# Optimization experiments

Hardware: AMD Instinct MI355X
Metric: run time of the kernel (lower is better)

## Reference

```python
import jax, jax.numpy as jnp
import numpy as np
import math

D_MODEL = 1024
N_HEADS = 16
D_HEAD = D_MODEL // N_HEADS
B, T = 2, 2048


def setup_inputs() -> dict:
    key = jax.random.key(0)
    ks = jax.random.split(key, 5)
    x = jax.random.normal(ks[0], (B, T, D_MODEL), dtype=jnp.float32)
    W_qkv = jax.random.normal(ks[1], (D_MODEL, 3 * D_MODEL), dtype=jnp.float32) * 0.02
    b_qkv = jnp.zeros((3 * D_MODEL,), dtype=jnp.float32)
    W_g = jax.random.normal(ks[2], (N_HEADS, D_HEAD, D_HEAD), dtype=jnp.float32) * 0.02
    W_out = jax.random.normal(ks[3], (D_MODEL, D_MODEL), dtype=jnp.float32) * 0.02
    b_out = jnp.zeros((D_MODEL,), dtype=jnp.float32)
    return {"x": x, "W_qkv": W_qkv, "b_qkv": b_qkv, "W_g": W_g, "W_out": W_out, "b_out": b_out}


def reference(x, W_qkv, b_qkv, W_g, W_out, b_out):
    b, t, d = x.shape
    h, dh = N_HEADS, D_HEAD
    qkv = x @ W_qkv + b_qkv                         # (B,T,3D)
    q, k, v = jnp.split(qkv, 3, axis=-1)
    # (B,T,D) -> (B,H,T,dh)
    q = q.reshape(b, t, h, dh).transpose(0, 2, 1, 3)
    k = k.reshape(b, t, h, dh).transpose(0, 2, 1, 3)
    v = v.reshape(b, t, h, dh).transpose(0, 2, 1, 3)
    scale = 1.0 / math.sqrt(dh)
    scores = jnp.einsum('bhtd,bhsd->bhts', q, k) * scale   # (B,H,T,T)
    causal = jnp.tril(jnp.ones((t, t), dtype=bool))
    scores = jnp.where(causal, scores, jnp.float32(-jnp.inf))
    attn = jax.nn.softmax(scores, axis=-1)
    # query-conditioned bilinear value gate (applied at each position)
    g = jax.nn.sigmoid(jnp.einsum('bhtd,hde->bhte', q, W_g))  # (B,H,T,dh)
    v = g * v
    out = jnp.einsum('bhts,bhsd->bhtd', attn, v)             # (B,H,T,dh)
    out = out.transpose(0, 2, 1, 3).reshape(b, t, d)
    return out @ W_out + b_out
```

## Files before the change

### kernel.cpp

```cpp
#include <hip/hip_runtime.h>
#include <hip/hip_bf16.h>

typedef unsigned short ushortT;
typedef __bf16 bf16x8 __attribute__((ext_vector_type(8)));
typedef __bf16 bf16x4 __attribute__((ext_vector_type(4)));
typedef float f32x4 __attribute__((ext_vector_type(4)));

#define T_SEQ 2048
#define DH 64
#define NH 16
#define DM 1024
#define TD 3072
#define BATCH 2
#define LOG2E 1.44269504f

#define BARRIER()   asm volatile("s_barrier" ::: "memory")
#define VMCNT(n)    asm volatile("s_waitcnt vmcnt(" #n ")" ::: "memory")

__device__ inline ushortT f2bf(float f){
    union { float f; unsigned int u; } a; a.f = f;
    unsigned int r = a.u + 0x7fffu + ((a.u >> 16) & 1u);
    return (ushortT)(r >> 16);
}
__device__ inline float bf2f(ushortT u){
    union { float f; unsigned int u; } a; a.u = ((unsigned int)u) << 16;
    return a.f;
}

__device__ inline void gload_lds16(const void* g, void* l){
    __builtin_amdgcn_global_load_lds((const __attribute__((address_space(1))) void*)g,
                                     (__attribute__((address_space(3))) void*)l, 16, 0, 0);
}

__global__ __launch_bounds__(256) void cast_bf16_kernel(const float* __restrict__ in,
                                                        ushortT* __restrict__ out, int n){
    int i = (blockIdx.x * 256 + threadIdx.x) * 4;
    if (i < n){
        float4 v = *(const float4*)&in[i];
        out[i+0] = f2bf(v.x); out[i+1] = f2bf(v.y);
        out[i+2] = f2bf(v.z); out[i+3] = f2bf(v.w);
    }
}

__global__ __launch_bounds__(256) void transcast_kernel(const float* __restrict__ in,
                                                        ushortT* __restrict__ out, int K, int N){
    __shared__ float tile[64][65];
    int n0 = blockIdx.x * 64, k0 = blockIdx.y * 64;
    int tid = threadIdx.x;
    int c  = tid & 63;
    int r4 = tid >> 6;
#pragma unroll
    for (int i = 0; i < 16; i++){
        int k = r4 + i * 4;
        tile[k][c] = in[(size_t)(k0 + k) * N + n0 + c];
    }
    __syncthreads();
#pragma unroll
    for (int i = 0; i < 16; i++){
        int n = r4 + i * 4;
        out[(size_t)(n0 + n) * K + k0 + c] = f2bf(tile[c][n]);
    }
}

__global__ __launch_bounds__(256) void wg_transcast_kernel(const float* __restrict__ in,
                                                           ushortT* __restrict__ out){
    __shared__ float tile[64][65];
    int h = blockIdx.x;
    int tid = threadIdx.x;
    int c = tid & 63, r4 = tid >> 6;
#pragma unroll
    for (int i = 0; i < 16; i++){
        int d = r4 + i*4;
        tile[d][c] = in[h*4096 + d*64 + c];
    }
    __syncthreads();
#pragma unroll
    for (int i = 0; i < 16; i++){
        int e = r4 + i*4;
        out[h*4096 + e*64 + c] = f2bf(tile[c][e]);
    }
}

__device__ inline void store_out(ushortT* C, size_t i, float v){ C[i] = f2bf(v); }
__device__ inline void store_out(float*   C, size_t i, float v){ C[i] = v; }

template <typename OUT>
__global__ __launch_bounds__(256) void gemm_bf16_kernel(const ushortT* __restrict__ A,
                                                        const ushortT* __restrict__ BT,
                                                        const float* __restrict__ bias,
                                                        OUT* __restrict__ C,
                                                        int M, int N, int K){
    __shared__ __align__(16) ushortT As[2][128*32];
    __shared__ __align__(16) ushortT Bs[2][128*32];
    int tid = threadIdx.x;
    int m0 = blockIdx.x * 128;
    int n0 = blockIdx.y * 128;
    int wid = tid >> 6, lane = tid & 63;
    int l15 = lane & 15, g = lane >> 4;
    int wr = wid >> 1, wc = wid & 1;

    f32x4 acc[4][4];
#pragma unroll
    for (int i = 0; i < 4; i++)
#pragma unroll
        for (int j = 0; j < 4; j++) acc[i][j] = (f32x4){0.f,0.f,0.f,0.f};

    int srow = wid * 32 + (lane >> 2);
    int sch  = lane & 3;

#define GSTAGE(buf, k0)                                                                  \
    {                                                                                    \
        _Pragma("unroll")                                                                \
        for (int i_ = 0; i_ < 2; i_++){                                                  \
            int row_ = srow + i_ * 16;                                                   \
            const ushortT* asrc_ = A  + (size_t)(m0 + row_) * K + (k0) + sch * 8;        \
            const ushortT* bsrc_ = BT + (size_t)(n0 + row_) * K + (k0) + sch * 8;        \
            gload_lds16(asrc_, (char*)As[buf] + (wid*2 + i_) * 1024);                    \
            gload_lds16(bsrc_, (char*)Bs[buf] + (wid*2 + i_) * 1024);                    \
        }                                                                                \
    }

    GSTAGE(0, 0);

    int nk = K >> 5;
    for (int kt = 0; kt < nk; kt++){
        int buf = kt & 1;
        BARRIER();
        if (kt + 1 < nk){
            GSTAGE(buf ^ 1, (kt + 1) * 32);
            VMCNT(4);
        } else {
            VMCNT(0);
        }
        BARRIER();

        bf16x8 af[4], bfr[4];
#pragma unroll
        for (int mi = 0; mi < 4; mi++){
            int r = wr*64 + mi*16 + l15;
            af[mi]  = *(const bf16x8*)(As[buf] + r*32 + g*8);
        }
#pragma unroll
        for (int ni = 0; ni < 4; ni++){
            int r = wc*64 + ni*16 + l15;
            bfr[ni] = *(const bf16x8*)(Bs[buf] + r*32 + g*8);
        }
#pragma unroll
        for (int mi = 0; mi < 4; mi++)
#pragma unroll
            for (int ni = 0; ni < 4; ni++)
                acc[mi][ni] = __builtin_amdgcn_mfma_f32_16x16x32_bf16(af[mi], bfr[ni], acc[mi][ni], 0, 0, 0);
    }
#undef GSTAGE

#pragma unroll
    for (int mi = 0; mi < 4; mi++){
#pragma unroll
        for (int jj = 0; jj < 4; jj++){
            int mm = m0 + wr*64 + mi*16 + 4*g + jj;
#pragma unroll
            for (int ni = 0; ni < 4; ni++){
                int nn = n0 + wc*64 + ni*16 + l15;
                float v = acc[mi][ni][jj] + bias[nn];
                store_out(C, (size_t)mm * N + nn, v);
            }
        }
    }
}

__global__ __launch_bounds__(256) void gate_kernel(const ushortT* __restrict__ qkv,
                                                   const ushortT* __restrict__ WgT,
                                                   ushortT* __restrict__ vgT){
    __shared__ __align__(16) ushortT VT[64][72];
    int tblk = blockIdx.x, bh = blockIdx.y;
    int b = bh >> 4, h = bh & 15;
    int tid = threadIdx.x, wid = tid >> 6, lane = tid & 63;
    int l15 = lane & 15, g = lane >> 4;
    int t0 = tblk * 64;
    int tl = wid*16 + l15;

    const ushortT* qrow = qkv + ((size_t)b*T_SEQ + t0 + tl)*TD + h*DH;
    bf16x8 qf0 = *(const bf16x8*)(qrow + 8*g);
    bf16x8 qf1 = *(const bf16x8*)(qrow + 32 + 8*g);

    const ushortT* wbase = WgT + h*4096;
    const ushortT* vrow = qkv + ((size_t)b*T_SEQ + t0 + tl)*TD + 2*DM + h*DH;

#pragma unroll
    for (int ns = 0; ns < 4; ns++){
        int e = ns*16 + l15;
        bf16x8 wf0 = *(const bf16x8*)(wbase + e*64 + 8*g);
        bf16x8 wf1 = *(const bf16x8*)(wbase + e*64 + 32 + 8*g);
        f32x4 z = (f32x4){0.f,0.f,0.f,0.f};
        z = __builtin_amdgcn_mfma_f32_16x16x32_bf16(wf0, qf0, z, 0, 0, 0);
        z = __builtin_amdgcn_mfma_f32_16x16x32_bf16(wf1, qf1, z, 0, 0, 0);
        union { ushortT u[4]; uint2 v; } v4;
        v4.v = *(const uint2*)(vrow + ns*16 + 4*g);
#pragma unroll
        for (int jj = 0; jj < 4; jj++){
            float ex = __builtin_amdgcn_exp2f(-z[jj] * LOG2E);
            float gv = __builtin_amdgcn_rcpf(1.f + ex);
            VT[ns*16 + 4*g + jj][tl] = f2bf(gv * bf2f(v4.u[jj]));
        }
    }
    __syncthreads();
    for (int i = tid; i < 64*8; i += 256){
        int e = i >> 3, c8 = (i & 7) * 8;
        *(uint4*)&vgT[((size_t)bh * DH + e) * T_SEQ + t0 + c8] = *(const uint4*)&VT[e][c8];
    }
}

struct QS {
    bf16x8 qf0, qf1;
    float m_, lsum;
    f32x4 acc[4];
};

__device__ __forceinline__ void proc2(const ushortT* __restrict__ K0,
                                      const ushortT* __restrict__ V0,
                                      const ushortT* __restrict__ K1,
                                      const ushortT* __restrict__ V1,
                                      QS& S, int t0, int t1, int myp,
                                      int wq, int l15, int g){
    int l7 = l15 & 7;
    f32x4 s[8];
    __builtin_amdgcn_s_setprio(1);
#pragma unroll
    for (int ns = 0; ns < 4; ns++){
        int kr = ns*16 + l15;
        bf16x8 kf0 = *(const bf16x8*)(K0 + kr*64 + ((g    ) ^ l7)*8);
        bf16x8 kf1 = *(const bf16x8*)(K0 + kr*64 + ((4 + g) ^ l7)*8);
        f32x4 z = (f32x4){0.f,0.f,0.f,0.f};
        z = __builtin_amdgcn_mfma_f32_16x16x32_bf16(kf0, S.qf0, z, 0, 0, 0);
        z = __builtin_amdgcn_mfma_f32_16x16x32_bf16(kf1, S.qf1, z, 0, 0, 0);
        s[ns] = z;
    }
#pragma unroll
    for (int ns = 0; ns < 4; ns++){
        int kr = ns*16 + l15;
        bf16x8 kf0 = *(const bf16x8*)(K1 + kr*64 + ((g    ) ^ l7)*8);
        bf16x8 kf1 = *(const bf16x8*)(K1 + kr*64 + ((4 + g) ^ l7)*8);
        f32x4 z = (f32x4){0.f,0.f,0.f,0.f};
        z = __builtin_amdgcn_mfma_f32_16x16x32_bf16(kf0, S.qf0, z, 0, 0, 0);
        z = __builtin_amdgcn_mfma_f32_16x16x32_bf16(kf1, S.qf1, z, 0, 0, 0);
        s[4 + ns] = z;
    }
    __builtin_amdgcn_s_setprio(0);

    int qrel = wq*16 + l15;
    bool diag0 = (t0 == myp);
    bool inv1  = (t1 > myp);
    bool diag1 = (t1 == myp);
    if (diag0){
#pragma unroll
        for (int ns = 0; ns < 4; ns++){
            int kb = ((ns & 2) << 4) + 8*g + ((ns & 1) << 2);
#pragma unroll
            for (int jj = 0; jj < 4; jj++)
                if (kb + jj > qrel) s[ns][jj] = -INFINITY;
        }
    }
    if (inv1){
#pragma unroll
        for (int ns = 0; ns < 4; ns++)
#pragma unroll
            for (int jj = 0; jj < 4; jj++) s[4+ns][jj] = -INFINITY;
    } else if (diag1){
#pragma unroll
        for (int ns = 0; ns < 4; ns++){
            int kb = ((ns & 2) << 4) + 8*g + ((ns & 1) << 2);
#pragma unroll
            for (int jj = 0; jj < 4; jj++)
                if (kb + jj > qrel) s[4+ns][jj] = -INFINITY;
        }
    }

    float tmax = -INFINITY;
#pragma unroll
    for (int ns = 0; ns < 8; ns++){
        float a = fmaxf(s[ns][0], s[ns][1]);
        float c = fmaxf(s[ns][2], s[ns][3]);
        tmax = fmaxf(tmax, fmaxf(a, c));
    }
    tmax = fmaxf(tmax, __shfl_xor(tmax, 16, 64));
    tmax = fmaxf(tmax, __shfl_xor(tmax, 32, 64));

    float mnew = fmaxf(S.m_, tmax);
    float mc = mnew * LOG2E;
    float rs = 0.f;
    bf16x8 pa[4];
#pragma unroll
    for (int pr = 0; pr < 4; pr++){
#pragma unroll
        for (int jj = 0; jj < 4; jj++){
            float p0 = __builtin_amdgcn_exp2f(fmaf(s[2*pr  ][jj], LOG2E, -mc));
            float p1 = __builtin_amdgcn_exp2f(fmaf(s[2*pr+1][jj], LOG2E, -mc));
            rs += p0 + p1;
            pa[pr][jj]   = (__bf16)p0;
            pa[pr][4+jj] = (__bf16)p1;
        }
    }
    rs += __shfl_xor(rs, 16, 64);
    rs += __shfl_xor(rs, 32, 64);

    if (!__all(mnew == S.m_)){
        float alpha = __builtin_amdgcn_exp2f(fmaf(S.m_, LOG2E, -mc));
#pragma unroll
        for (int nt = 0; nt < 4; nt++)
#pragma unroll
            for (int jj = 0; jj < 4; jj++) S.acc[nt][jj] *= alpha;
        S.lsum *= alpha;
        S.m_ = mnew;
    }
    S.lsum += rs;

    __builtin_amdgcn_s_setprio(1);
#pragma unroll
    for (int ks = 0; ks < 2; ks++){
#pragma unroll
        for (int nt = 0; nt < 4; nt++){
            bf16x8 vf = *(const bf16x8*)(V0 + (nt*16 + l15)*64 + ((ks*4 + g) ^ l7)*8);
            S.acc[nt] = __builtin_amdgcn_mfma_f32_16x16x32_bf16(vf, pa[ks], S.acc[nt], 0, 0, 0);
        }
    }
    if (!inv1){
#pragma unroll
        for (int ks = 0; ks < 2; ks++){
#pragma unroll
            for (int nt = 0; nt < 4; nt++){
                bf16x8 vf = *(const bf16x8*)(V1 + (nt*16 + l15)*64 + ((ks*4 + g) ^ l7)*8);
                S.acc[nt] = __builtin_amdgcn_mfma_f32_16x16x32_bf16(vf, pa[2+ks], S.acc[nt], 0, 0, 0);
            }
        }
    }
    __builtin_amdgcn_s_setprio(0);
}

__global__ __launch_bounds__(512, 2) void attn_kernel(const ushortT* __restrict__ qkv,
                                                      const ushortT* __restrict__ vgT,
                                                      ushortT* __restrict__ obf){
    __shared__ __align__(16) ushortT Ks[2][2][64*64];
    __shared__ __align__(16) ushortT Vs[2][2][64*64];
    int bh = blockIdx.x, y = blockIdx.y;
    int pairid = (y < 8) ? y : 23 - y;
    int b = bh >> 4, h = bh & 15;
    int tid = threadIdx.x, wid = tid >> 6, lane = tid & 63;
    int l15 = lane & 15, g = lane >> 4;
    int grp = wid >> 2;
    int wq  = wid & 3;

    const ushortT* Kg = qkv + (size_t)b * T_SEQ * TD + DM + h * DH;
    const ushortT* Vg = vgT + (size_t)bh * DH * T_SEQ;

    int pA = pairid, pB = 31 - pairid;
    int myp = grp ? pB : pA;

    int st_row  = tid >> 3;
    int st_c    = (tid & 7) ^ (st_row & 7);
    int st_prow = (st_row & 0x20) | ((st_row & 0x0C) << 1) |
                  ((st_row & 0x10) >> 2) | (st_row & 3);

#define STAGE_ROUND(buf, rr)                                                             \
    {                                                                                    \
        int t0_ = 2*(rr);     if (t0_ > pB) t0_ = pB;                                    \
        int t1_ = 2*(rr) + 1; if (t1_ > pB) t1_ = pB;                                    \
        gload_lds16(Kg + (size_t)(t0_*64 + st_prow) * TD + st_c*8,                       \
                    (char*)Ks[buf][0] + tid*16);                                         \
        gload_lds16(Kg + (size_t)(t1_*64 + st_prow) * TD + st_c*8,                       \
                    (char*)Ks[buf][1] + tid*16);                                         \
        gload_lds16(Vg + (size_t)st_row * T_SEQ + t0_*64 + st_c*8,                       \
                    (char*)Vs[buf][0] + tid*16);                                         \
        gload_lds16(Vg + (size_t)st_row * T_SEQ + t1_*64 + st_c*8,                       \
                    (char*)Vs[buf][1] + tid*16);                                         \
    }

    QS S;
    {
        int qrow = myp*64 + wq*16 + l15;
        const ushortT* qb = qkv + ((size_t)b * T_SEQ + qrow) * TD + h * DH;
        S.qf0 = *(const bf16x8*)(qb + 8*g);
        S.qf1 = *(const bf16x8*)(qb + 32 + 8*g);
#pragma unroll
        for (int j = 0; j < 8; j++){
            S.qf0[j] = (__bf16)((float)S.qf0[j] * 0.125f);
            S.qf1[j] = (__bf16)((float)S.qf1[j] * 0.125f);
        }
        S.m_ = -INFINITY; S.lsum = 0.f;
#pragma unroll
        for (int nt = 0; nt < 4; nt++) S.acc[nt] = (f32x4){0.f,0.f,0.f,0.f};
    }

    int nr = (33 - pairid) >> 1;
    STAGE_ROUND(0, 0);

    for (int r = 0; r < nr; r++){
        int buf = r & 1;
        BARRIER();
        if (r + 1 < nr){
            STAGE_ROUND(buf ^ 1, r + 1);
            VMCNT(4);
        } else {
            VMCNT(0);
        }
        BARRIER();
        int t0 = 2*r;
        if (t0 <= myp)
            proc2(Ks[buf][0], Vs[buf][0], Ks[buf][1], Vs[buf][1],
                  S, t0, t0 + 1, myp, wq, l15, g);
    }
#undef STAGE_ROUND

    float inv = 1.f / S.lsum;
    size_t orow = ((size_t)b * T_SEQ + myp*64 + wq*16 + l15) * DM + h*DH;
#pragma unroll
    for (int nt = 0; nt < 4; nt++){
        union { ushortT u[4]; uint2 v; } pk;
#pragma unroll
        for (int jj = 0; jj < 4; jj++) pk.u[jj] = f2bf(S.acc[nt][jj] * inv);
        *(uint2*)&obf[orow + nt*16 + 4*g] = pk.v;
    }
}

extern "C" void kernel_launch(void* const* d_in, const int* in_sizes, int n_in,
                              void* d_out, int out_size, void* d_ws, size_t ws_size,
                              hipStream_t stream){
    const float* x    = (const float*)d_in[0];
    const float* Wqkv = (const float*)d_in[1];
    const float* bqkv = (const float*)d_in[2];
    const float* Wg   = (const float*)d_in[3];
    const float* Wout = (const float*)d_in[4];
    const float* bout = (const float*)d_in[5];

    char* ws = (char*)d_ws;
    ushortT* xbf   = (ushortT*)(ws);
    ushortT* wqkvT = (ushortT*)(ws + 8388608);
    ushortT* woutT = (ushortT*)(ws + 14680064);
    ushortT* qkvb  = (ushortT*)(ws + 16777216);
    ushortT* vgT   = (ushortT*)(ws + 41943040);
    ushortT* obf   = (ushortT*)(ws + 50331648);
    ushortT* wgT   = (ushortT*)(ws + 58720256);

    cast_bf16_kernel<<<4096, 256, 0, stream>>>(x, xbf, 4194304);
    transcast_kernel<<<dim3(48,16), 256, 0, stream>>>(Wqkv, wqkvT, 1024, 3072);
    transcast_kernel<<<dim3(16,16), 256, 0, stream>>>(Wout, woutT, 1024, 1024);
    wg_transcast_kernel<<<16, 256, 0, stream>>>(Wg, wgT);
    gemm_bf16_kernel<ushortT><<<dim3(32,24), 256, 0, stream>>>(xbf, wqkvT, bqkv, qkvb, 4096, 3072, 1024);
    gate_kernel<<<dim3(32,32), 256, 0, stream>>>(qkvb, wgT, vgT);
    attn_kernel<<<dim3(32,16), 512, 0, stream>>>(qkvb, vgT, obf);
    gemm_bf16_kernel<float><<<dim3(32,8), 256, 0, stream>>>(obf, woutT, bout, (float*)d_out, 4096, 1024, 1024);
}
```

Baseline: 118.9 us.

## Give each attention wave two query tiles and merge prep kernels into one launch

The attention kernel now runs 256 threads per block instead of 512, and each wave handles two 16-row query tiles. This lets every K and V fragment read from LDS feed two MFMAs, halving LDS fragment traffic per unit of compute. In exchange, per-thread registers grow (scores and accumulators are doubled), there are fewer waves to hide latency, and each thread now issues twice as many staging loads. Separately, the four input cast/transpose kernels are merged into one launch to remove launch overhead.

```diff
diff --git a/kernel.cpp b/kernel.cpp
--- a/kernel.cpp
+++ b/kernel.cpp
@@ -3,7 +3,6 @@
 
 typedef unsigned short ushortT;
 typedef __bf16 bf16x8 __attribute__((ext_vector_type(8)));
-typedef __bf16 bf16x4 __attribute__((ext_vector_type(4)));
 typedef float f32x4 __attribute__((ext_vector_type(4)));
 
 #define T_SEQ 2048
@@ -32,23 +31,47 @@
                                      (__attribute__((address_space(3))) void*)l, 16, 0, 0);
 }
 
-__global__ __launch_bounds__(256) void cast_bf16_kernel(const float* __restrict__ in,
-                                                        ushortT* __restrict__ out, int n){
-    int i = (blockIdx.x * 256 + threadIdx.x) * 4;
-    if (i < n){
-        float4 v = *(const float4*)&in[i];
-        out[i+0] = f2bf(v.x); out[i+1] = f2bf(v.y);
-        out[i+2] = f2bf(v.z); out[i+3] = f2bf(v.w);
-    }
-}
-
-__global__ __launch_bounds__(256) void transcast_kernel(const float* __restrict__ in,
-                                                        ushortT* __restrict__ out, int K, int N){
+__global__ __launch_bounds__(256) void prep_kernel(const float* __restrict__ x,
+                                                   ushortT* __restrict__ xbf,
+                                                   const float* __restrict__ Wqkv,
+                                                   ushortT* __restrict__ wqkvT,
+                                                   const float* __restrict__ Wout,
+                                                   ushortT* __restrict__ woutT,
+                                                   const float* __restrict__ Wg,
+                                                   ushortT* __restrict__ wgT){
     __shared__ float tile[64][65];
-    int n0 = blockIdx.x * 64, k0 = blockIdx.y * 64;
-    int tid = threadIdx.x;
-    int c  = tid & 63;
-    int r4 = tid >> 6;
+    int blk = blockIdx.x, tid = threadIdx.x;
+    if (blk < 4096){
+        int i = (blk * 256 + tid) * 4;
+        float4 v = *(const float4*)&x[i];
+        xbf[i+0] = f2bf(v.x); xbf[i+1] = f2bf(v.y);
+        xbf[i+2] = f2bf(v.z); xbf[i+3] = f2bf(v.w);
+        return;
+    }
+    int c = tid & 63, r4 = tid >> 6;
+    if (blk >= 5120){
+        int h = blk - 5120;
+#pragma unroll
+        for (int i = 0; i < 16; i++){
+            int d = r4 + i*4;
+            tile[d][c] = Wg[h*4096 + d*64 + c];
+        }
+        __syncthreads();
+#pragma unroll
+        for (int i = 0; i < 16; i++){
+            int e = r4 + i*4;
+            wgT[h*4096 + e*64 + c] = f2bf(tile[c][e]);
+        }
+        return;
+    }
+    const float* in; ushortT* out; int K, N, n0, k0;
+    if (blk < 4864){
+        int t = blk - 4096; in = Wqkv; out = wqkvT; K = 1024; N = 3072;
+        n0 = (t % 48) * 64; k0 = (t / 48) * 64;
+    } else {
+        int t = blk - 4864; in = Wout; out = woutT; K = 1024; N = 1024;
+        n0 = (t & 15) * 64; k0 = (t >> 4) * 64;
+    }
 #pragma unroll
     for (int i = 0; i < 16; i++){
         int k = r4 + i * 4;
@@ -59,25 +82,6 @@
     for (int i = 0; i < 16; i++){
         int n = r4 + i * 4;
         out[(size_t)(n0 + n) * K + k0 + c] = f2bf(tile[c][n]);
-    }
-}
-
-__global__ __launch_bounds__(256) void wg_transcast_kernel(const float* __restrict__ in,
-                                                           ushortT* __restrict__ out){
-    __shared__ float tile[64][65];
-    int h = blockIdx.x;
-    int tid = threadIdx.x;
-    int c = tid & 63, r4 = tid >> 6;
-#pragma unroll
-    for (int i = 0; i < 16; i++){
-        int d = r4 + i*4;
-        tile[d][c] = in[h*4096 + d*64 + c];
-    }
-    __syncthreads();
-#pragma unroll
-    for (int i = 0; i < 16; i++){
-        int e = r4 + i*4;
-        out[h*4096 + e*64 + c] = f2bf(tile[c][e]);
     }
 }
 
@@ -210,133 +214,131 @@
     }
 }
 
-struct QS {
-    bf16x8 qf0, qf1;
-    float m_, lsum;
-    f32x4 acc[4];
+struct QS2 {
+    bf16x8 qf[2][2];
+    float m_[2], lsum[2];
+    f32x4 acc[2][4];
 };
 
-__device__ __forceinline__ void proc2(const ushortT* __restrict__ K0,
-                                      const ushortT* __restrict__ V0,
-                                      const ushortT* __restrict__ K1,
-                                      const ushortT* __restrict__ V1,
-                                      QS& S, int t0, int t1, int myp,
-                                      int wq, int l15, int g){
+__device__ __forceinline__ void proc2x(const ushortT* __restrict__ K0,
+                                       const ushortT* __restrict__ V0,
+                                       const ushortT* __restrict__ K1,
+                                       const ushortT* __restrict__ V1,
+                                       QS2& S, int t0, int t1, int myp,
+                                       int half, int l15, int g){
     int l7 = l15 & 7;
-    f32x4 s[8];
+    f32x4 s[2][8];
     __builtin_amdgcn_s_setprio(1);
 #pragma unroll
-    for (int ns = 0; ns < 4; ns++){
-        int kr = ns*16 + l15;
-        bf16x8 kf0 = *(const bf16x8*)(K0 + kr*64 + ((g    ) ^ l7)*8);
-        bf16x8 kf1 = *(const bf16x8*)(K0 + kr*64 + ((4 + g) ^ l7)*8);
-        f32x4 z = (f32x4){0.f,0.f,0.f,0.f};
-        z = __builtin_amdgcn_mfma_f32_16x16x32_bf16(kf0, S.qf0, z, 0, 0, 0);
-        z = __builtin_amdgcn_mfma_f32_16x16x32_bf16(kf1, S.qf1, z, 0, 0, 0);
-        s[ns] = z;
-    }
-#pragma unroll
-    for (int ns = 0; ns < 4; ns++){
-        int kr = ns*16 + l15;
-        bf16x8 kf0 = *(const bf16x8*)(K1 + kr*64 + ((g    ) ^ l7)*8);
-        bf16x8 kf1 = *(const bf16x8*)(K1 + kr*64 + ((4 + g) ^ l7)*8);
-        f32x4 z = (f32x4){0.f,0.f,0.f,0.f};
-        z = __builtin_amdgcn_mfma_f32_16x16x32_bf16(kf0, S.qf0, z, 0, 0, 0);
-        z = __builtin_amdgcn_mfma_f32_16x16x32_bf16(kf1, S.qf1, z, 0, 0, 0);
-        s[4 + ns] = z;
+    for (int T = 0; T < 2; T++){
+        const ushortT* Kb = T ? K1 : K0;
+#pragma unroll
+        for (int ns = 0; ns < 4; ns++){
+            int kr = ns*16 + l15;
+            bf16x8 kf0 = *(const bf16x8*)(Kb + kr*64 + ((g    ) ^ l7)*8);
+            bf16x8 kf1 = *(const bf16x8*)(Kb + kr*64 + ((4 + g) ^ l7)*8);
+#pragma unroll
+            for (int mi = 0; mi < 2; mi++){
+                f32x4 z = (f32x4){0.f,0.f,0.f,0.f};
+                z = __builtin_amdgcn_mfma_f32_16x16x32_bf16(kf0, S.qf[mi][0], z, 0, 0, 0);
+                z = __builtin_amdgcn_mfma_f32_16x16x32_bf16(kf1, S.qf[mi][1], z, 0, 0, 0);
+                s[mi][T*4 + ns] = z;
+            }
+        }
     }
     __builtin_amdgcn_s_setprio(0);
 
-    int qrel = wq*16 + l15;
     bool diag0 = (t0 == myp);
     bool inv1  = (t1 > myp);
     bool diag1 = (t1 == myp);
-    if (diag0){
-#pragma unroll
-        for (int ns = 0; ns < 4; ns++){
-            int kb = ((ns & 2) << 4) + 8*g + ((ns & 1) << 2);
-#pragma unroll
-            for (int jj = 0; jj < 4; jj++)
-                if (kb + jj > qrel) s[ns][jj] = -INFINITY;
-        }
-    }
-    if (inv1){
-#pragma unroll
-        for (int ns = 0; ns < 4; ns++)
-#pragma unroll
-            for (int jj = 0; jj < 4; jj++) s[4+ns][jj] = -INFINITY;
-    } else if (diag1){
-#pragma unroll
-        for (int ns = 0; ns < 4; ns++){
-            int kb = ((ns & 2) << 4) + 8*g + ((ns & 1) << 2);
-#pragma unroll
-            for (int jj = 0; jj < 4; jj++)
-                if (kb + jj > qrel) s[4+ns][jj] = -INFINITY;
-        }
-    }
-
-    float tmax = -INFINITY;
-#pragma unroll
-    for (int ns = 0; ns < 8; ns++){
-        float a = fmaxf(s[ns][0], s[ns][1]);
-        float c = fmaxf(s[ns][2], s[ns][3]);
-        tmax = fmaxf(tmax, fmaxf(a, c));
-    }
-    tmax = fmaxf(tmax, __shfl_xor(tmax, 16, 64));
-    tmax = fmaxf(tmax, __shfl_xor(tmax, 32, 64));
-
-    float mnew = fmaxf(S.m_, tmax);
-    float mc = mnew * LOG2E;
-    float rs = 0.f;
-    bf16x8 pa[4];
-#pragma unroll
-    for (int pr = 0; pr < 4; pr++){
-#pragma unroll
-        for (int jj = 0; jj < 4; jj++){
-            float p0 = __builtin_amdgcn_exp2f(fmaf(s[2*pr  ][jj], LOG2E, -mc));
-            float p1 = __builtin_amdgcn_exp2f(fmaf(s[2*pr+1][jj], LOG2E, -mc));
-            rs += p0 + p1;
-            pa[pr][jj]   = (__bf16)p0;
-            pa[pr][4+jj] = (__bf16)p1;
-        }
-    }
-    rs += __shfl_xor(rs, 16, 64);
-    rs += __shfl_xor(rs, 32, 64);
-
-    if (!__all(mnew == S.m_)){
-        float alpha = __builtin_amdgcn_exp2f(fmaf(S.m_, LOG2E, -mc));
-#pragma unroll
-        for (int nt = 0; nt < 4; nt++)
-#pragma unroll
-            for (int jj = 0; jj < 4; jj++) S.acc[nt][jj] *= alpha;
-        S.lsum *= alpha;
-        S.m_ = mnew;
-    }
-    S.lsum += rs;
+    bf16x8 pa[2][4];
+#pragma unroll
+    for (int mi = 0; mi < 2; mi++){
+        int qrel = half*32 + mi*16 + l15;
+        if (diag0){
+#pragma unroll
+            for (int ns = 0; ns < 4; ns++){
+                int kb = ((ns & 2) << 4) + 8*g + ((ns & 1) << 2);
+#pragma unroll
+                for (int jj = 0; jj < 4; jj++)
+                    if (kb + jj > qrel) s[mi][ns][jj] = -INFINITY;
+            }
+        }
+        if (inv1){
+#pragma unroll
+            for (int ns = 0; ns < 4; ns++)
+#pragma unroll
+                for (int jj = 0; jj < 4; jj++) s[mi][4+ns][jj] = -INFINITY;
+        } else if (diag1){
+#pragma unroll
+            for (int ns = 0; ns < 4; ns++){
+                int kb = ((ns & 2) << 4) + 8*g + ((ns & 1) << 2);
+#pragma unroll
+                for (int jj = 0; jj < 4; jj++)
+                    if (kb + jj > qrel) s[mi][4+ns][jj] = -INFINITY;
+            }
+        }
+
+        float tmax = -INFINITY;
+#pragma unroll
+        for (int ns = 0; ns < 8; ns++){
+            float a = fmaxf(s[mi][ns][0], s[mi][ns][1]);
+            float c = fmaxf(s[mi][ns][2], s[mi][ns][3]);
+            tmax = fmaxf(tmax, fmaxf(a, c));
+        }
+        tmax = fmaxf(tmax, __shfl_xor(tmax, 16, 64));
+        tmax = fmaxf(tmax, __shfl_xor(tmax, 32, 64));
+
+        float mnew = fmaxf(S.m_[mi], tmax);
+        float mc = mnew * LOG2E;
+        float rs = 0.f;
+#pragma unroll
+        for (int pr = 0; pr < 4; pr++){
+#pragma unroll
+            for (int jj = 0; jj < 4; jj++){
+                float p0 = __builtin_amdgcn_exp2f(fmaf(s[mi][2*pr  ][jj], LOG2E, -mc));
+                float p1 = __builtin_amdgcn_exp2f(fmaf(s[mi][2*pr+1][jj], LOG2E, -mc));
+                rs += p0 + p1;
+                pa[mi][pr][jj]   = (__bf16)p0;
+                pa[mi][pr][4+jj] = (__bf16)p1;
+            }
+        }
+        rs += __shfl_xor(rs, 16, 64);
+        rs += __shfl_xor(rs, 32, 64);
+
+        if (!__all(mnew == S.m_[mi])){
+            float alpha = __builtin_amdgcn_exp2f(fmaf(S.m_[mi], LOG2E, -mc));
+#pragma unroll
+            for (int nt = 0; nt < 4; nt++)
+#pragma unroll
+                for (int jj = 0; jj < 4; jj++) S.acc[mi][nt][jj] *= alpha;
+            S.lsum[mi] *= alpha;
+            S.m_[mi] = mnew;
+        }
+        S.lsum[mi] += rs;
+    }
 
     __builtin_amdgcn_s_setprio(1);
 #pragma unroll
-    for (int ks = 0; ks < 2; ks++){
-#pragma unroll
-        for (int nt = 0; nt < 4; nt++){
-            bf16x8 vf = *(const bf16x8*)(V0 + (nt*16 + l15)*64 + ((ks*4 + g) ^ l7)*8);
-            S.acc[nt] = __builtin_amdgcn_mfma_f32_16x16x32_bf16(vf, pa[ks], S.acc[nt], 0, 0, 0);
-        }
-    }
-    if (!inv1){
+    for (int T = 0; T < 2; T++){
+        if (T == 1 && inv1) break;
+        const ushortT* Vb = T ? V1 : V0;
 #pragma unroll
         for (int ks = 0; ks < 2; ks++){
 #pragma unroll
             for (int nt = 0; nt < 4; nt++){
-                bf16x8 vf = *(const bf16x8*)(V1 + (nt*16 + l15)*64 + ((ks*4 + g) ^ l7)*8);
-                S.acc[nt] = __builtin_amdgcn_mfma_f32_16x16x32_bf16(vf, pa[2+ks], S.acc[nt], 0, 0, 0);
+                bf16x8 vf = *(const bf16x8*)(Vb + (nt*16 + l15)*64 + ((ks*4 + g) ^ l7)*8);
+#pragma unroll
+                for (int mi = 0; mi < 2; mi++)
+                    S.acc[mi][nt] = __builtin_amdgcn_mfma_f32_16x16x32_bf16(
+                        vf, pa[mi][T*2 + ks], S.acc[mi][nt], 0, 0, 0);
             }
         }
     }
     __builtin_amdgcn_s_setprio(0);
 }
 
-__global__ __launch_bounds__(512, 2) void attn_kernel(const ushortT* __restrict__ qkv,
+__global__ __launch_bounds__(256, 2) void attn_kernel(const ushortT* __restrict__ qkv,
                                                       const ushortT* __restrict__ vgT,
                                                       ushortT* __restrict__ obf){
     __shared__ __align__(16) ushortT Ks[2][2][64*64];
@@ -346,8 +348,8 @@
     int b = bh >> 4, h = bh & 15;
     int tid = threadIdx.x, wid = tid >> 6, lane = tid & 63;
     int l15 = lane & 15, g = lane >> 4;
-    int grp = wid >> 2;
-    int wq  = wid & 3;
+    int grp  = wid >> 1;
+    int half = wid & 1;
 
     const ushortT* Kg = qkv + (size_t)b * T_SEQ * TD + DM + h * DH;
     const ushortT* Vg = vgT + (size_t)bh * DH * T_SEQ;
@@ -355,39 +357,45 @@
     int pA = pairid, pB = 31 - pairid;
     int myp = grp ? pB : pA;
 
-    int st_row  = tid >> 3;
-    int st_c    = (tid & 7) ^ (st_row & 7);
-    int st_prow = (st_row & 0x20) | ((st_row & 0x0C) << 1) |
-                  ((st_row & 0x10) >> 2) | (st_row & 3);
+    int sr0 = tid >> 3;
+    int sc0 = tid & 7;
 
 #define STAGE_ROUND(buf, rr)                                                             \
     {                                                                                    \
         int t0_ = 2*(rr);     if (t0_ > pB) t0_ = pB;                                    \
         int t1_ = 2*(rr) + 1; if (t1_ > pB) t1_ = pB;                                    \
-        gload_lds16(Kg + (size_t)(t0_*64 + st_prow) * TD + st_c*8,                       \
-                    (char*)Ks[buf][0] + tid*16);                                         \
-        gload_lds16(Kg + (size_t)(t1_*64 + st_prow) * TD + st_c*8,                       \
-                    (char*)Ks[buf][1] + tid*16);                                         \
-        gload_lds16(Vg + (size_t)st_row * T_SEQ + t0_*64 + st_c*8,                       \
-                    (char*)Vs[buf][0] + tid*16);                                         \
-        gload_lds16(Vg + (size_t)st_row * T_SEQ + t1_*64 + st_c*8,                       \
-                    (char*)Vs[buf][1] + tid*16);                                         \
-    }
-
-    QS S;
-    {
-        int qrow = myp*64 + wq*16 + l15;
+        _Pragma("unroll")                                                                \
+        for (int i_ = 0; i_ < 2; i_++){                                                  \
+            int row_  = sr0 + i_*32;                                                     \
+            int sc_   = sc0 ^ (row_ & 7);                                                \
+            int prow_ = (row_ & 0x20) | ((row_ & 0x0C) << 1) |                           \
+                        ((row_ & 0x10) >> 2) | (row_ & 3);                               \
+            gload_lds16(Kg + (size_t)(t0_*64 + prow_) * TD + sc_*8,                      \
+                        (char*)Ks[buf][0] + tid*16 + i_*4096);                           \
+            gload_lds16(Kg + (size_t)(t1_*64 + prow_) * TD + sc_*8,                      \
+                        (char*)Ks[buf][1] + tid*16 + i_*4096);                           \
+            gload_lds16(Vg + (size_t)row_ * T_SEQ + t0_*64 + sc_*8,                      \
+                        (char*)Vs[buf][0] + tid*16 + i_*4096);                           \
+            gload_lds16(Vg + (size_t)row_ * T_SEQ + t1_*64 + sc_*8,                      \
+                        (char*)Vs[buf][1] + tid*16 + i_*4096);                           \
+        }                                                                                \
+    }
+
+    QS2 S;
+#pragma unroll
+    for (int mi = 0; mi < 2; mi++){
+        int qrow = myp*64 + half*32 + mi*16 + l15;
         const ushortT* qb = qkv + ((size_t)b * T_SEQ + qrow) * TD + h * DH;
-        S.qf0 = *(const bf16x8*)(qb + 8*g);
-        S.qf1 = *(const bf16x8*)(qb + 32 + 8*g);
+        S.qf[mi][0] = *(const bf16x8*)(qb + 8*g);
+        S.qf[mi][1] = *(const bf16x8*)(qb + 32 + 8*g);
 #pragma unroll
         for (int j = 0; j < 8; j++){
-            S.qf0[j] = (__bf16)((float)S.qf0[j] * 0.125f);
-            S.qf1[j] = (__bf16)((float)S.qf1[j] * 0.125f);
-        }
-        S.m_ = -INFINITY; S.lsum = 0.f;
-#pragma unroll
-        for (int nt = 0; nt < 4; nt++) S.acc[nt] = (f32x4){0.f,0.f,0.f,0.f};
+            S.qf[mi][0][j] = (__bf16)((float)S.qf[mi][0][j] * 0.125f);
+            S.qf[mi][1][j] = (__bf16)((float)S.qf[mi][1][j] * 0.125f);
+        }
+        S.m_[mi] = -INFINITY; S.lsum[mi] = 0.f;
+#pragma unroll
+        for (int nt = 0; nt < 4; nt++) S.acc[mi][nt] = (f32x4){0.f,0.f,0.f,0.f};
     }
 
     int nr = (33 - pairid) >> 1;
@@ -398,26 +406,29 @@
         BARRIER();
         if (r + 1 < nr){
             STAGE_ROUND(buf ^ 1, r + 1);
-            VMCNT(4);
+            VMCNT(8);
         } else {
             VMCNT(0);
         }
         BARRIER();
         int t0 = 2*r;
         if (t0 <= myp)
-            proc2(Ks[buf][0], Vs[buf][0], Ks[buf][1], Vs[buf][1],
-                  S, t0, t0 + 1, myp, wq, l15, g);
+            proc2x(Ks[buf][0], Vs[buf][0], Ks[buf][1], Vs[buf][1],
+                   S, t0, t0 + 1, myp, half, l15, g);
     }
 #undef STAGE_ROUND
 
-    float inv = 1.f / S.lsum;
-    size_t orow = ((size_t)b * T_SEQ + myp*64 + wq*16 + l15) * DM + h*DH;
-#pragma unroll
-    for (int nt = 0; nt < 4; nt++){
-        union { ushortT u[4]; uint2 v; } pk;
-#pragma unroll
-        for (int jj = 0; jj < 4; jj++) pk.u[jj] = f2bf(S.acc[nt][jj] * inv);
-        *(uint2*)&obf[orow + nt*16 + 4*g] = pk.v;
+#pragma unroll
+    for (int mi = 0; mi < 2; mi++){
+        float inv = 1.f / S.lsum[mi];
+        size_t orow = ((size_t)b * T_SEQ + myp*64 + half*32 + mi*16 + l15) * DM + h*DH;
+#pragma unroll
+        for (int nt = 0; nt < 4; nt++){
+            union { ushortT u[4]; uint2 v; } pk;
+#pragma unroll
+            for (int jj = 0; jj < 4; jj++) pk.u[jj] = f2bf(S.acc[mi][nt][jj] * inv);
+            *(uint2*)&obf[orow + nt*16 + 4*g] = pk.v;
+        }
     }
 }
 
@@ -440,12 +451,9 @@
     ushortT* obf   = (ushortT*)(ws + 50331648);
     ushortT* wgT   = (ushortT*)(ws + 58720256);
 
-    cast_bf16_kernel<<<4096, 256, 0, stream>>>(x, xbf, 4194304);
-    transcast_kernel<<<dim3(48,16), 256, 0, stream>>>(Wqkv, wqkvT, 1024, 3072);
-    transcast_kernel<<<dim3(16,16), 256, 0, stream>>>(Wout, woutT, 1024, 1024);
-    wg_transcast_kernel<<<16, 256, 0, stream>>>(Wg, wgT);
+    prep_kernel<<<5136, 256, 0, stream>>>(x, xbf, Wqkv, wqkvT, Wout, woutT, Wg, wgT);
     gemm_bf16_kernel<ushortT><<<dim3(32,24), 256, 0, stream>>>(xbf, wqkvT, bqkv, qkvb, 4096, 3072, 1024);
     gate_kernel<<<dim3(32,32), 256, 0, stream>>>(qkvb, wgT, vgT);
-    attn_kernel<<<dim3(32,16), 512, 0, stream>>>(qkvb, vgT, obf);
+    attn_kernel<<<dim3(32,16), 256, 0, stream>>>(qkvb, vgT, obf);
     gemm_bf16_kernel<float><<<dim3(32,8), 256, 0, stream>>>(obf, woutT, bout, (float*)d_out, 4096, 1024, 1024);
 }
```

Result: slower. 123.6 us (+4.0%).
